# Performance work log

Hardware: AMD Instinct MI355X
Metric: run time of the kernel (lower is better)

## Reference

```python
import jax, jax.numpy as jnp
import numpy as np

B, Cin, Cout, H, W, K = 8, 256, 256, 64, 64, 3  # kernel 3x3, stride 1, pad 1, dilation 1
EPS = 1e-5


def setup_inputs() -> dict:
    key = jax.random.key(0)
    k0, k1, k2 = jax.random.split(key, 3)
    x = jax.random.normal(k0, (B, Cin, H, W), jnp.float32)
    # offset-predicting conv (mmcv zero-inits it; use small random weights so offsets are nontrivial)
    w_off = jax.random.normal(k1, (2 * K * K, Cin, K, K), jnp.float32) * 0.01
    b_off = jnp.zeros((2 * K * K,), jnp.float32)
    # main deformable conv weight
    w = jax.random.normal(k2, (Cout, Cin, K, K), jnp.float32) * (1.0 / np.sqrt(Cin * K * K))
    b = jnp.zeros((Cout,), jnp.float32)
    gamma = jnp.ones((Cout,), jnp.float32)
    beta = jnp.zeros((Cout,), jnp.float32)
    return {"x": x, "w_off": w_off, "b_off": b_off, "w": w, "b": b, "gamma": gamma, "beta": beta}


def _deform_fusion(x, w_off, b_off, w, b, gamma, beta):
    Bn, C, Hh, Ww = x.shape
    # 1) predict offsets: [B, 2*K*K, H, W]; channel layout is (dy, dx) per kernel tap
    offset = jax.lax.conv_general_dilated(x, w_off, (1, 1), ((1, 1), (1, 1)))
    offset = offset + b_off[None, :, None, None]
    off = offset.reshape(Bn, K * K, 2, Hh, Ww)
    dy, dx = off[:, :, 0], off[:, :, 1]  # each [B, K*K, H, W]

    # 2) sampling positions: p = p0 + p_k + delta_p  (stride 1, pad 1 -> p_k in {-1,0,1})
    kk = jnp.arange(K * K)
    ky = (kk // K - (K // 2)).astype(jnp.float32)[None, :, None, None]
    kx = (kk % K - (K // 2)).astype(jnp.float32)[None, :, None, None]
    py = ky + jnp.arange(Hh, dtype=jnp.float32)[None, None, :, None] + dy  # [B,K2,H,W]
    px = kx + jnp.arange(Ww, dtype=jnp.float32)[None, None, None, :] + dx

    # 3) bilinear sampling with zero padding outside the image
    y0 = jnp.floor(py); x0 = jnp.floor(px)
    fy = py - y0; fx = px - x0
    x_flat = x.reshape(Bn, C, Hh * Ww)

    def corner(yi, xi, wgt):
        valid = (yi >= 0) & (yi <= Hh - 1) & (xi >= 0) & (xi <= Ww - 1)
        idx = (jnp.clip(yi, 0, Hh - 1) * Ww + jnp.clip(xi, 0, Ww - 1)).astype(jnp.int32)
        idx = idx.reshape(Bn, -1)  # [B, K2*H*W]
        g = jax.vmap(lambda xf, ii: jnp.take(xf, ii, axis=1))(x_flat, idx)  # [B,C,K2*H*W]
        return g * (wgt * valid).reshape(Bn, 1, -1)

    sampled = (corner(y0,     x0,     (1 - fy) * (1 - fx))
             + corner(y0,     x0 + 1, (1 - fy) * fx)
             + corner(y0 + 1, x0,     fy * (1 - fx))
             + corner(y0 + 1, x0 + 1, fy * fx))  # [B, C, K2*H*W]
    sampled = sampled.reshape(Bn, C, K * K, Hh * Ww)

    # 4) contract sampled patches with conv weight: implicit-GEMM of deformable conv
    out = jnp.einsum('bckp,ock->bop', sampled, w.reshape(w.shape[0], C, K * K))
    out = out + b[None, :, None]
    out = out.reshape(Bn, -1, Hh, Ww)

    # 5) BatchNorm (training-mode batch statistics) + ReLU
    mean = out.mean(axis=(0, 2, 3), keepdims=True)
    var = out.var(axis=(0, 2, 3), keepdims=True)
    out = gamma[None, :, None, None] * (out - mean) * jax.lax.rsqrt(var + EPS) + beta[None, :, None, None]
    return jax.nn.relu(out)


def reference(x, w_off, b_off, w, b, gamma, beta):
    return _deform_fusion(x, w_off, b_off, w, b, gamma, beta)
```

## Files before the change

### kernel.cpp

```cpp
#include <hip/hip_runtime.h>
#include <math.h>

#define BN_ 8
#define CIN 256
#define COUT 256
#define HH 64
#define WW 64
#define HW 4096
#define KK 9
#define OC 18
#define EPS 1e-5f
#define NTOT (BN_ * COUT * HW)

#define OFF_WS 0
#define WTB_WS 589824
#define WOB_WS 884736
#define ST_WS  921600
#define XT_WS  922112

typedef float f32x4 __attribute__((ext_vector_type(4)));
typedef float f32x2 __attribute__((ext_vector_type(2)));
typedef short s16x8 __attribute__((ext_vector_type(8)));
typedef unsigned int u32x4 __attribute__((ext_vector_type(4)));

__device__ __forceinline__ unsigned short f2bf(float f) {
  unsigned int u = __float_as_uint(f);
  unsigned int r = (u + 0x7fffu + ((u >> 16) & 1u)) >> 16;
  return (unsigned short)r;
}
__device__ __forceinline__ float bf2f(short s) {
  return __uint_as_float(((unsigned int)(unsigned short)s) << 16);
}

__global__ __launch_bounds__(256) void xpose_kernel(
    const float* __restrict__ x, unsigned short* __restrict__ xt) {
  __shared__ float s[64][65];
  const int t = threadIdx.x;
  const int p0 = blockIdx.x * 64;
  const int c0 = blockIdx.y * 64;
  const int b  = blockIdx.z;
  const float* xb = x + ((size_t)b * CIN + c0) * HW + p0;
#pragma unroll
  for (int pass = 0; pass < 4; ++pass) {
    int cr = pass * 16 + (t >> 4);
    int ps = (t & 15) * 4;
    float4 v = *(const float4*)(xb + (size_t)cr * HW + ps);
    s[ps + 0][cr] = v.x; s[ps + 1][cr] = v.y; s[ps + 2][cr] = v.z; s[ps + 3][cr] = v.w;
  }
  __syncthreads();
  unsigned short* xo = xt + (size_t)b * 32 * HW * 8;
#pragma unroll
  for (int r = 0; r < 2; ++r) {
    int flat = r * 256 + t;
    int pr = flat >> 3, sub = flat & 7;
    int g8 = (c0 >> 3) + sub;
    s16x8 v;
#pragma unroll
    for (int j = 0; j < 8; ++j) v[j] = (short)f2bf(s[pr][sub * 8 + j]);
    *(s16x8*)(xo + ((size_t)g8 * HW + p0 + pr) * 8) = v;
  }
}

__global__ __launch_bounds__(256) void prep_kernel(
    const float* __restrict__ w_off, const float* __restrict__ w,
    unsigned short* __restrict__ wob, unsigned short* __restrict__ wTb,
    float* __restrict__ stats) {
  const int kb = blockIdx.x;
  const int kk = kb >> 3;
  const int c0 = (kb & 7) << 5;
  const int t = threadIdx.x;
  if (kb == 71) { stats[t] = 0.f; stats[256 + t] = 0.f; }
#pragma unroll
  for (int r = 0; r < 4; ++r) {
    int e = r * 256 + t;
    int g = e >> 8, m = (e >> 3) & 31, j = e & 7;
    int c = c0 + g * 8 + j;
    unsigned short v = 0;
    if (m < OC) v = f2bf(w_off[((size_t)m * CIN + c) * 9 + kk]);
    wob[(size_t)kb * 1024 + e] = v;
  }
#pragma unroll
  for (int g = 0; g < 4; ++g)
#pragma unroll
    for (int j = 0; j < 8; ++j) {
      int c = c0 + g * 8 + j;
      wTb[(((size_t)kb * 4 + g) * 256 + t) * 8 + j] =
          f2bf(w[((size_t)t * CIN + c) * 9 + kk]);
    }
}

__global__ __launch_bounds__(256) void offset_kernel(
    const unsigned short* __restrict__ xt, const unsigned short* __restrict__ wob,
    const float* __restrict__ b_off, float* __restrict__ off_ws) {
  __shared__ __align__(16) char smem[32768];
  const int t = threadIdx.x;
  const int lane = t & 63;
  const int wv = t >> 6;
  const int b = blockIdx.x & 7;
  const int h = blockIdx.x >> 3;
  const unsigned short* xtb = xt + (size_t)b * 32 * HW * 8;
  const int fr = lane & 15, fq = lane >> 4;
  unsigned short* sb = (unsigned short*)smem + wv * 2048;
  float* red = (float*)smem;

  f32x4 acc[2][4] = {};

  for (int s = 0; s < 18; ++s) {
    const int ki = wv * 18 + s;
    const int kk = ki >> 3, cc0 = (ki & 7) << 5;
    const int ky = kk / 3 - 1, kx = kk % 3 - 1;
    const int y = h + ky;
    const bool yok = (y >= 0) && (y < HH);
    const int xcol = lane + kx;
    const bool ok = yok && (xcol >= 0) && (xcol < WW);
    const int pix = y * WW + xcol;

    s16x8 af[2];
    const unsigned short* ap = wob + (size_t)ki * 1024;
#pragma unroll
    for (int i = 0; i < 2; ++i)
      af[i] = *(const s16x8*)&ap[(fq * 32 + i * 16 + fr) * 8];

#pragma unroll
    for (int g = 0; g < 4; ++g) {
      s16x8 v = {0, 0, 0, 0, 0, 0, 0, 0};
      if (ok)
        __builtin_memcpy(&v, (const char*)xtb + ((((size_t)(cc0 >> 3) + g) << 16)) + (size_t)pix * 16, 16);
      *(s16x8*)&sb[(g * 64 + lane) * 8] = v;
    }
    __builtin_amdgcn_s_waitcnt(0);

    s16x8 bf[4];
#pragma unroll
    for (int jn = 0; jn < 4; ++jn)
      bf[jn] = *(const s16x8*)&sb[(fq * 64 + jn * 16 + fr) * 8];
#pragma unroll
    for (int i = 0; i < 2; ++i)
#pragma unroll
      for (int jn = 0; jn < 4; ++jn)
        acc[i][jn] = __builtin_amdgcn_mfma_f32_16x16x32_bf16(af[i], bf[jn], acc[i][jn], 0, 0, 0);
  }

  __syncthreads();
#pragma unroll
  for (int i = 0; i < 2; ++i)
#pragma unroll
    for (int jn = 0; jn < 4; ++jn)
#pragma unroll
      for (int rg = 0; rg < 4; ++rg)
        red[wv * 2048 + (i * 16 + fq * 4 + rg) * 64 + jn * 16 + fr] = acc[i][jn][rg];
  __syncthreads();

  const int m = t >> 3;
  const int pq = (t & 7) * 8;
  float4 v0 = make_float4(0.f, 0.f, 0.f, 0.f), v1 = v0;
#pragma unroll
  for (int w = 0; w < 4; ++w) {
    float4 a = *(float4*)&red[w * 2048 + m * 64 + pq];
    float4 c = *(float4*)&red[w * 2048 + m * 64 + pq + 4];
    v0.x += a.x; v0.y += a.y; v0.z += a.z; v0.w += a.w;
    v1.x += c.x; v1.y += c.y; v1.z += c.z; v1.w += c.w;
  }
  if (m < OC) {
    float bo = b_off[m];
    v0.x += bo; v0.y += bo; v0.z += bo; v0.w += bo;
    v1.x += bo; v1.y += bo; v1.z += bo; v1.w += bo;
    float* op = off_ws + ((size_t)b * OC + m) * HW + h * WW + pq;
    *(float4*)op = v0;
    *(float4*)(op + 4) = v1;
  }
}

__global__ __launch_bounds__(512, 4) void gemm_kernel(
    const unsigned short* __restrict__ xt, const unsigned short* __restrict__ wTb,
    const float* __restrict__ off_ws, const float* __restrict__ bias,
    float* __restrict__ out, float* __restrict__ stats) {
  __shared__ unsigned short s_b[2][4096];
  const int t = threadIdx.x;
  const int lane = t & 63;
  const int wv = t >> 6;
  const int b = blockIdx.x & 7;
  const int h = blockIdx.x >> 3;
  const int p0 = h * 64;
  const int col = t & 63;
  const int oct = t >> 6;
  const int fr = lane & 15, fq = lane >> 4;
  const unsigned short* xtb = xt + (size_t)b * 32 * HW * 8;
  const float* offp = off_ws + (size_t)b * OC * HW + p0 + col;

  int cofs[4];
  f32x2 qw2[4];

  auto calc = [&](int kk, float dy, float dx) {
    float py = (float)(kk / 3 - 1 + h) + dy;
    float pxx = (float)(kk % 3 - 1 + col) + dx;
    float y0f = floorf(py), x0f = floorf(pxx);
    float fy = py - y0f, fx = pxx - x0f;
    int y0 = (int)y0f, x0 = (int)x0f;
    int y1 = y0 + 1, x1 = x0 + 1;
    bool vy0 = (y0 >= 0) && (y0 < HH), vy1 = (y1 >= 0) && (y1 < HH);
    bool vx0 = (x0 >= 0) && (x0 < WW), vx1 = (x1 >= 0) && (x1 < WW);
    int cy0 = min(max(y0, 0), HH - 1), cy1 = min(max(y1, 0), HH - 1);
    int cx0 = min(max(x0, 0), WW - 1), cx1 = min(max(x1, 0), WW - 1);
    float q0 = (vy0 && vx0) ? (1.f - fy) * (1.f - fx) : 0.f;
    float q1 = (vy0 && vx1) ? (1.f - fy) * fx : 0.f;
    float q2 = (vy1 && vx0) ? fy * (1.f - fx) : 0.f;
    float q3 = (vy1 && vx1) ? fy * fx : 0.f;
    cofs[0] = (cy0 * WW + cx0) * 16;  qw2[0][0] = q0; qw2[0][1] = q0;
    cofs[1] = (cy0 * WW + cx1) * 16;  qw2[1][0] = q1; qw2[1][1] = q1;
    cofs[2] = (cy1 * WW + cx0) * 16;  qw2[2][0] = q2; qw2[2][1] = q2;
    cofs[3] = (cy1 * WW + cx1) * 16;  qw2[3][0] = q3; qw2[3][1] = q3;
  };

  s16x8 g[4];

  auto gather = [&](int chunk64) {
    const char* bp = (const char*)xtb + (((size_t)(chunk64 * 8 + oct)) << 16);
#pragma unroll
    for (int k = 0; k < 4; ++k)
      __builtin_memcpy(&g[k], bp + cofs[k], 16);
  };

  auto combine_write = [&](int buf) {
    u32x4 vout;
#pragma unroll
    for (int jp = 0; jp < 4; ++jp) {
      f32x2 a = {0.f, 0.f};
#pragma unroll
      for (int k = 0; k < 4; ++k) {
        unsigned int pr = ((const unsigned int*)&g[k])[jp];
        f32x2 xv;
        xv[0] = __uint_as_float(pr << 16);
        xv[1] = __uint_as_float(pr & 0xffff0000u);
        a = __builtin_elementwise_fma(qw2[k], xv, a);
      }
      unsigned int packed;
      asm("v_cvt_pk_bf16_f32 %0, %1, %2" : "=v"(packed) : "v"(a[0]), "v"(a[1]));
      vout[jp] = packed;
    }
    *(u32x4*)&s_b[buf][(oct * 64 + col) * 8] = vout;
  };

  auto load_a = [&](int iter, s16x8 af[2][2]) {
#pragma unroll
    for (int ks = 0; ks < 2; ++ks) {
      const unsigned short* ap =
          wTb + (((size_t)(iter * 2 + ks) * 4 + fq) * 256 + wv * 32 + fr) * 8;
#pragma unroll
      for (int i = 0; i < 2; ++i)
        af[ks][i] = *(const s16x8*)(ap + (size_t)i * 16 * 8);
    }
  };

  f32x4 acc[2][4] = {};
  s16x8 afE[2][2], afO[2][2];
  float dyp, dxp;

  {
    float dy0 = offp[0];
    float dx0 = offp[HW];
    calc(0, dy0, dx0);
    dyp = offp[2 * HW];
    dxp = offp[3 * HW];
    gather(0);
    load_a(0, afE);
    combine_write(0);
  }
  asm volatile("s_waitcnt lgkmcnt(0)" ::: "memory");
  __builtin_amdgcn_s_barrier();

#define GBODY(I, AFC, AFN, CUR)                                                \
  {                                                                            \
    const int nx1 = (I) + 1;                                                   \
    if (nx1 < 36) {                                                            \
      if ((nx1 & 3) == 0) {                                                    \
        const int kkc = nx1 >> 2;                                              \
        calc(kkc, dyp, dxp);                                                   \
        const int kkn = kkc + 1;                                               \
        if (kkn < 9) {                                                         \
          dyp = offp[(size_t)(2 * kkn) * HW];                                  \
          dxp = offp[(size_t)(2 * kkn + 1) * HW];                              \
        }                                                                      \
      }                                                                        \
      gather(nx1 & 3);                                                         \
      load_a(nx1, AFN);                                                        \
    }                                                                          \
    __builtin_amdgcn_s_setprio(1);                                             \
    _Pragma("unroll")                                                          \
    for (int ks = 0; ks < 2; ++ks)                                             \
      _Pragma("unroll")                                                        \
      for (int jj = 0; jj < 4; ++jj) {                                         \
        s16x8 bfr = *(const s16x8*)&s_b[CUR][((ks * 4 + fq) * 64 + jj * 16 + fr) * 8]; \
        _Pragma("unroll")                                                      \
        for (int ii = 0; ii < 2; ++ii)                                         \
          acc[ii][jj] = __builtin_amdgcn_mfma_f32_16x16x32_bf16(               \
              AFC[ks][ii], bfr, acc[ii][jj], 0, 0, 0);                         \
      }                                                                        \
    __builtin_amdgcn_s_setprio(0);                                             \
    if (nx1 < 36) {                                                            \
      combine_write((CUR) ^ 1);                                                \
      asm volatile("s_waitcnt lgkmcnt(0)" ::: "memory");                       \
      __builtin_amdgcn_s_barrier();                                            \
    }                                                                          \
  }

  for (int m = 0; m < 18; ++m) {
    const int i0 = 2 * m;
    GBODY(i0, afE, afO, 0)
    GBODY(i0 + 1, afO, afE, 1)
  }
#undef GBODY

#pragma unroll
  for (int i = 0; i < 2; ++i) {
#pragma unroll
    for (int rg = 0; rg < 4; ++rg) {
      int o = wv * 32 + i * 16 + fq * 4 + rg;
      float bv = bias[o];
      float* op = out + ((size_t)(b * COUT + o)) * HW + p0 + fr;
      float s = 0.f, s2 = 0.f;
#pragma unroll
      for (int j = 0; j < 4; ++j) {
        float val = acc[i][j][rg] + bv;
        op[j * 16] = val;
        s += val; s2 += val * val;
      }
#pragma unroll
      for (int m2 = 1; m2 < 16; m2 <<= 1) {
        s += __shfl_xor(s, m2);
        s2 += __shfl_xor(s2, m2);
      }
      if (fr == 0) {
        atomicAdd(&stats[o], s);
        atomicAdd(&stats[COUT + o], s2);
      }
    }
  }
}

__global__ __launch_bounds__(256) void bn_kernel(
    float* __restrict__ out, const float* __restrict__ stats,
    const float* __restrict__ gamma, const float* __restrict__ beta) {
  int i4 = (blockIdx.x * 256 + threadIdx.x) * 4;
  int o = (i4 >> 12) & (COUT - 1);
  const float inv_n = 1.f / (float)(BN_ * HW);
  float mean = stats[o] * inv_n;
  float var = stats[COUT + o] * inv_n - mean * mean;
  float sc = gamma[o] * rsqrtf(var + EPS);
  float sh = beta[o] - mean * sc;
  float4 v = *(float4*)(out + i4);
  v.x = fmaxf(fmaf(v.x, sc, sh), 0.f);
  v.y = fmaxf(fmaf(v.y, sc, sh), 0.f);
  v.z = fmaxf(fmaf(v.z, sc, sh), 0.f);
  v.w = fmaxf(fmaf(v.w, sc, sh), 0.f);
  *(float4*)(out + i4) = v;
}

extern "C" void kernel_launch(void* const* d_in, const int* in_sizes, int n_in,
                              void* d_out, int out_size, void* d_ws, size_t ws_size,
                              hipStream_t stream) {
  const float* x     = (const float*)d_in[0];
  const float* w_off = (const float*)d_in[1];
  const float* b_off = (const float*)d_in[2];
  const float* w     = (const float*)d_in[3];
  const float* bias  = (const float*)d_in[4];
  const float* gamma = (const float*)d_in[5];
  const float* beta  = (const float*)d_in[6];
  float* out = (float*)d_out;
  float* ws = (float*)d_ws;
  float* off_ws = ws + OFF_WS;
  unsigned short* wTb = (unsigned short*)(ws + WTB_WS);
  unsigned short* wob = (unsigned short*)(ws + WOB_WS);
  float* stats = ws + ST_WS;
  unsigned short* xt = (unsigned short*)(ws + XT_WS);

  xpose_kernel<<<dim3(64, 4, 8), 256, 0, stream>>>(x, xt);
  prep_kernel<<<72, 256, 0, stream>>>(w_off, w, wob, wTb, stats);
  offset_kernel<<<512, 256, 0, stream>>>(xt, wob, b_off, off_ws);
  gemm_kernel<<<512, 512, 0, stream>>>(xt, wTb, off_ws, bias, out, stats);
  bn_kernel<<<NTOT / 1024, 256, 0, stream>>>(out, stats, gamma, beta);
}
```

Before: 221.3 us.

## Warp-specialize GEMM kernel into MFMA consumer waves and gather producer waves

Splits the 8 waves of each block into 4 compute waves, which run the MFMA loop with a larger 64-row tile each, and 4 producer waves, which do the bilinear gather and bf16 packing into the double-buffered LDS tile. Previously every wave both gathered and computed. The aim is to overlap the irregular gather latency with matrix work through producer/consumer specialization. In exchange, each compute wave holds twice the accumulators and A fragments, which raises register pressure, and each producer handles two channel slots.

```diff
diff --git a/kernel.cpp b/kernel.cpp
--- a/kernel.cpp
+++ b/kernel.cpp
@@ -182,158 +182,164 @@
   const int b = blockIdx.x & 7;
   const int h = blockIdx.x >> 3;
   const int p0 = h * 64;
-  const int col = t & 63;
-  const int oct = t >> 6;
   const int fr = lane & 15, fq = lane >> 4;
   const unsigned short* xtb = xt + (size_t)b * 32 * HW * 8;
-  const float* offp = off_ws + (size_t)b * OC * HW + p0 + col;
-
-  int cofs[4];
-  f32x2 qw2[4];
-
-  auto calc = [&](int kk, float dy, float dx) {
-    float py = (float)(kk / 3 - 1 + h) + dy;
-    float pxx = (float)(kk % 3 - 1 + col) + dx;
-    float y0f = floorf(py), x0f = floorf(pxx);
-    float fy = py - y0f, fx = pxx - x0f;
-    int y0 = (int)y0f, x0 = (int)x0f;
-    int y1 = y0 + 1, x1 = x0 + 1;
-    bool vy0 = (y0 >= 0) && (y0 < HH), vy1 = (y1 >= 0) && (y1 < HH);
-    bool vx0 = (x0 >= 0) && (x0 < WW), vx1 = (x1 >= 0) && (x1 < WW);
-    int cy0 = min(max(y0, 0), HH - 1), cy1 = min(max(y1, 0), HH - 1);
-    int cx0 = min(max(x0, 0), WW - 1), cx1 = min(max(x1, 0), WW - 1);
-    float q0 = (vy0 && vx0) ? (1.f - fy) * (1.f - fx) : 0.f;
-    float q1 = (vy0 && vx1) ? (1.f - fy) * fx : 0.f;
-    float q2 = (vy1 && vx0) ? fy * (1.f - fx) : 0.f;
-    float q3 = (vy1 && vx1) ? fy * fx : 0.f;
-    cofs[0] = (cy0 * WW + cx0) * 16;  qw2[0][0] = q0; qw2[0][1] = q0;
-    cofs[1] = (cy0 * WW + cx1) * 16;  qw2[1][0] = q1; qw2[1][1] = q1;
-    cofs[2] = (cy1 * WW + cx0) * 16;  qw2[2][0] = q2; qw2[2][1] = q2;
-    cofs[3] = (cy1 * WW + cx1) * 16;  qw2[3][0] = q3; qw2[3][1] = q3;
-  };
-
-  s16x8 g[4];
-
-  auto gather = [&](int chunk64) {
-    const char* bp = (const char*)xtb + (((size_t)(chunk64 * 8 + oct)) << 16);
-#pragma unroll
-    for (int k = 0; k < 4; ++k)
-      __builtin_memcpy(&g[k], bp + cofs[k], 16);
-  };
-
-  auto combine_write = [&](int buf) {
-    u32x4 vout;
-#pragma unroll
-    for (int jp = 0; jp < 4; ++jp) {
-      f32x2 a = {0.f, 0.f};
+
+  if (wv < 4) {
+    f32x4 acc[4][4] = {};
+    s16x8 af[2][4];
+
+    auto load_af = [&](int iter) {
+#pragma unroll
+      for (int ks = 0; ks < 2; ++ks) {
+        const unsigned short* ap =
+            wTb + (((size_t)(iter * 2 + ks) * 4 + fq) * 256 + wv * 64 + fr) * 8;
+#pragma unroll
+        for (int i = 0; i < 4; ++i)
+          af[ks][i] = *(const s16x8*)(ap + (size_t)i * 16 * 8);
+      }
+    };
+
+    load_af(0);
+    asm volatile("s_waitcnt lgkmcnt(0)" ::: "memory");
+    __builtin_amdgcn_s_barrier();
+
+    for (int I = 0; I < 36; ++I) {
+      const int cur = I & 1;
+      __builtin_amdgcn_s_setprio(1);
+#pragma unroll
+      for (int ks = 0; ks < 2; ++ks)
+#pragma unroll
+        for (int jj = 0; jj < 4; ++jj) {
+          s16x8 bfr = *(const s16x8*)&s_b[cur][((ks * 4 + fq) * 64 + jj * 16 + fr) * 8];
+#pragma unroll
+          for (int ii = 0; ii < 4; ++ii)
+            acc[ii][jj] = __builtin_amdgcn_mfma_f32_16x16x32_bf16(
+                af[ks][ii], bfr, acc[ii][jj], 0, 0, 0);
+        }
+      __builtin_amdgcn_s_setprio(0);
+      if (I + 1 < 36) load_af(I + 1);
+      asm volatile("s_waitcnt lgkmcnt(0)" ::: "memory");
+      __builtin_amdgcn_s_barrier();
+    }
+
+#pragma unroll
+    for (int i = 0; i < 4; ++i) {
+#pragma unroll
+      for (int rg = 0; rg < 4; ++rg) {
+        int o = wv * 64 + i * 16 + fq * 4 + rg;
+        float bv = bias[o];
+        float* op = out + ((size_t)(b * COUT + o)) * HW + p0 + fr;
+        float s = 0.f, s2 = 0.f;
+#pragma unroll
+        for (int j = 0; j < 4; ++j) {
+          float val = acc[i][j][rg] + bv;
+          op[j * 16] = val;
+          s += val; s2 += val * val;
+        }
+#pragma unroll
+        for (int m2 = 1; m2 < 16; m2 <<= 1) {
+          s += __shfl_xor(s, m2);
+          s2 += __shfl_xor(s2, m2);
+        }
+        if (fr == 0) {
+          atomicAdd(&stats[o], s);
+          atomicAdd(&stats[COUT + o], s2);
+        }
+      }
+    }
+  } else {
+    const int col = lane;
+    const int octp = wv & 3;
+    const float* offp = off_ws + (size_t)b * OC * HW + p0 + col;
+
+    int cofs[4];
+    f32x2 qw2[4];
+    s16x8 g[2][4];
+
+    auto calc = [&](int kk, float dy, float dx) {
+      float py = (float)(kk / 3 - 1 + h) + dy;
+      float pxx = (float)(kk % 3 - 1 + col) + dx;
+      float y0f = floorf(py), x0f = floorf(pxx);
+      float fy = py - y0f, fx = pxx - x0f;
+      int y0 = (int)y0f, x0 = (int)x0f;
+      int y1 = y0 + 1, x1 = x0 + 1;
+      bool vy0 = (y0 >= 0) && (y0 < HH), vy1 = (y1 >= 0) && (y1 < HH);
+      bool vx0 = (x0 >= 0) && (x0 < WW), vx1 = (x1 >= 0) && (x1 < WW);
+      int cy0 = min(max(y0, 0), HH - 1), cy1 = min(max(y1, 0), HH - 1);
+      int cx0 = min(max(x0, 0), WW - 1), cx1 = min(max(x1, 0), WW - 1);
+      float q0 = (vy0 && vx0) ? (1.f - fy) * (1.f - fx) : 0.f;
+      float q1 = (vy0 && vx1) ? (1.f - fy) * fx : 0.f;
+      float q2 = (vy1 && vx0) ? fy * (1.f - fx) : 0.f;
+      float q3 = (vy1 && vx1) ? fy * fx : 0.f;
+      cofs[0] = (cy0 * WW + cx0) * 16;  qw2[0][0] = q0; qw2[0][1] = q0;
+      cofs[1] = (cy0 * WW + cx1) * 16;  qw2[1][0] = q1; qw2[1][1] = q1;
+      cofs[2] = (cy1 * WW + cx0) * 16;  qw2[2][0] = q2; qw2[2][1] = q2;
+      cofs[3] = (cy1 * WW + cx1) * 16;  qw2[3][0] = q3; qw2[3][1] = q3;
+    };
+
+    auto gather = [&](int chunk64) {
+      const char* bp0 = (const char*)xtb + (((size_t)(chunk64 * 8 + octp * 2)) << 16);
 #pragma unroll
       for (int k = 0; k < 4; ++k) {
-        unsigned int pr = ((const unsigned int*)&g[k])[jp];
-        f32x2 xv;
-        xv[0] = __uint_as_float(pr << 16);
-        xv[1] = __uint_as_float(pr & 0xffff0000u);
-        a = __builtin_elementwise_fma(qw2[k], xv, a);
-      }
-      unsigned int packed;
-      asm("v_cvt_pk_bf16_f32 %0, %1, %2" : "=v"(packed) : "v"(a[0]), "v"(a[1]));
-      vout[jp] = packed;
-    }
-    *(u32x4*)&s_b[buf][(oct * 64 + col) * 8] = vout;
-  };
-
-  auto load_a = [&](int iter, s16x8 af[2][2]) {
-#pragma unroll
-    for (int ks = 0; ks < 2; ++ks) {
-      const unsigned short* ap =
-          wTb + (((size_t)(iter * 2 + ks) * 4 + fq) * 256 + wv * 32 + fr) * 8;
-#pragma unroll
-      for (int i = 0; i < 2; ++i)
-        af[ks][i] = *(const s16x8*)(ap + (size_t)i * 16 * 8);
-    }
-  };
-
-  f32x4 acc[2][4] = {};
-  s16x8 afE[2][2], afO[2][2];
-  float dyp, dxp;
-
-  {
-    float dy0 = offp[0];
-    float dx0 = offp[HW];
-    calc(0, dy0, dx0);
-    dyp = offp[2 * HW];
-    dxp = offp[3 * HW];
-    gather(0);
-    load_a(0, afE);
-    combine_write(0);
-  }
-  asm volatile("s_waitcnt lgkmcnt(0)" ::: "memory");
-  __builtin_amdgcn_s_barrier();
-
-#define GBODY(I, AFC, AFN, CUR)                                                \
-  {                                                                            \
-    const int nx1 = (I) + 1;                                                   \
-    if (nx1 < 36) {                                                            \
-      if ((nx1 & 3) == 0) {                                                    \
-        const int kkc = nx1 >> 2;                                              \
-        calc(kkc, dyp, dxp);                                                   \
-        const int kkn = kkc + 1;                                               \
-        if (kkn < 9) {                                                         \
-          dyp = offp[(size_t)(2 * kkn) * HW];                                  \
-          dxp = offp[(size_t)(2 * kkn + 1) * HW];                              \
-        }                                                                      \
-      }                                                                        \
-      gather(nx1 & 3);                                                         \
-      load_a(nx1, AFN);                                                        \
-    }                                                                          \
-    __builtin_amdgcn_s_setprio(1);                                             \
-    _Pragma("unroll")                                                          \
-    for (int ks = 0; ks < 2; ++ks)                                             \
-      _Pragma("unroll")                                                        \
-      for (int jj = 0; jj < 4; ++jj) {                                         \
-        s16x8 bfr = *(const s16x8*)&s_b[CUR][((ks * 4 + fq) * 64 + jj * 16 + fr) * 8]; \
-        _Pragma("unroll")                                                      \
-        for (int ii = 0; ii < 2; ++ii)                                         \
-          acc[ii][jj] = __builtin_amdgcn_mfma_f32_16x16x32_bf16(               \
-              AFC[ks][ii], bfr, acc[ii][jj], 0, 0, 0);                         \
-      }                                                                        \
-    __builtin_amdgcn_s_setprio(0);                                             \
-    if (nx1 < 36) {                                                            \
-      combine_write((CUR) ^ 1);                                                \
-      asm volatile("s_waitcnt lgkmcnt(0)" ::: "memory");                       \
-      __builtin_amdgcn_s_barrier();                                            \
-    }                                                                          \
-  }
-
-  for (int m = 0; m < 18; ++m) {
-    const int i0 = 2 * m;
-    GBODY(i0, afE, afO, 0)
-    GBODY(i0 + 1, afO, afE, 1)
-  }
-#undef GBODY
-
-#pragma unroll
-  for (int i = 0; i < 2; ++i) {
-#pragma unroll
-    for (int rg = 0; rg < 4; ++rg) {
-      int o = wv * 32 + i * 16 + fq * 4 + rg;
-      float bv = bias[o];
-      float* op = out + ((size_t)(b * COUT + o)) * HW + p0 + fr;
-      float s = 0.f, s2 = 0.f;
-#pragma unroll
-      for (int j = 0; j < 4; ++j) {
-        float val = acc[i][j][rg] + bv;
-        op[j * 16] = val;
-        s += val; s2 += val * val;
-      }
-#pragma unroll
-      for (int m2 = 1; m2 < 16; m2 <<= 1) {
-        s += __shfl_xor(s, m2);
-        s2 += __shfl_xor(s2, m2);
-      }
-      if (fr == 0) {
-        atomicAdd(&stats[o], s);
-        atomicAdd(&stats[COUT + o], s2);
-      }
+        __builtin_memcpy(&g[0][k], bp0 + cofs[k], 16);
+        __builtin_memcpy(&g[1][k], bp0 + (1 << 16) + cofs[k], 16);
+      }
+    };
+
+    auto combine_write = [&](int buf) {
+#pragma unroll
+      for (int slot = 0; slot < 2; ++slot) {
+        u32x4 vout;
+#pragma unroll
+        for (int jp = 0; jp < 4; ++jp) {
+          f32x2 a = {0.f, 0.f};
+#pragma unroll
+          for (int k = 0; k < 4; ++k) {
+            unsigned int pr = ((const unsigned int*)&g[slot][k])[jp];
+            f32x2 xv;
+            xv[0] = __uint_as_float(pr << 16);
+            xv[1] = __uint_as_float(pr & 0xffff0000u);
+            a = __builtin_elementwise_fma(qw2[k], xv, a);
+          }
+          unsigned int packed;
+          asm("v_cvt_pk_bf16_f32 %0, %1, %2" : "=v"(packed) : "v"(a[0]), "v"(a[1]));
+          vout[jp] = packed;
+        }
+        *(u32x4*)&s_b[buf][((octp * 2 + slot) * 64 + col) * 8] = vout;
+      }
+    };
+
+    float dyp, dxp;
+    {
+      float dy0 = offp[0];
+      float dx0 = offp[HW];
+      calc(0, dy0, dx0);
+      dyp = offp[2 * HW];
+      dxp = offp[3 * HW];
+      gather(0);
+      combine_write(0);
+    }
+    asm volatile("s_waitcnt lgkmcnt(0)" ::: "memory");
+    __builtin_amdgcn_s_barrier();
+
+    for (int I = 0; I < 36; ++I) {
+      const int nx1 = I + 1;
+      if (nx1 < 36) {
+        if ((nx1 & 3) == 0) {
+          const int kkc = nx1 >> 2;
+          calc(kkc, dyp, dxp);
+          const int kkn = kkc + 1;
+          if (kkn < 9) {
+            dyp = offp[(size_t)(2 * kkn) * HW];
+            dxp = offp[(size_t)(2 * kkn + 1) * HW];
+          }
+        }
+        gather(nx1 & 3);
+        combine_write((I & 1) ^ 1);
+      }
+      asm volatile("s_waitcnt lgkmcnt(0)" ::: "memory");
+      __builtin_amdgcn_s_barrier();
     }
   }
 }
```

Result: no change. 223.5 us (+1.0%).

## Fuse BatchNorm+ReLU into GEMM via grid barrier; prefetch offset-conv operands

Applied to the files above, without the earlier changes.

The separate bn_kernel pass is removed. The GEMM kernel now accumulates per-channel statistics, waits on a software grid-wide barrier (an atomic counter placed in a padding slot of the offset-weight buffer), and then applies the normalisation, bias and ReLU directly to its register accumulators before the only store of the output. This avoids writing the pre-BN output and then reading and rewriting it. The offset kernel is also software-pipelined: the global loads for the next step are issued before the current step's LDS reads and MFMAs. The barrier assumes all 512 blocks are resident at once, and it relies on prep_kernel resetting the padding slot on every call.

```diff
diff --git a/kernel.cpp b/kernel.cpp
--- a/kernel.cpp
+++ b/kernel.cpp
@@ -105,41 +105,53 @@
 
   f32x4 acc[2][4] = {};
 
-  for (int s = 0; s < 18; ++s) {
+  auto fetch = [&](int s, s16x8* V, s16x8* AF) {
     const int ki = wv * 18 + s;
-    const int kk = ki >> 3, cc0 = (ki & 7) << 5;
+    const int kk = ki >> 3, cc0g = (ki & 7) << 2;
     const int ky = kk / 3 - 1, kx = kk % 3 - 1;
     const int y = h + ky;
-    const bool yok = (y >= 0) && (y < HH);
     const int xcol = lane + kx;
-    const bool ok = yok && (xcol >= 0) && (xcol < WW);
+    const bool ok = (y >= 0) && (y < HH) && (xcol >= 0) && (xcol < WW);
     const int pix = y * WW + xcol;
-
-    s16x8 af[2];
-    const unsigned short* ap = wob + (size_t)ki * 1024;
-#pragma unroll
-    for (int i = 0; i < 2; ++i)
-      af[i] = *(const s16x8*)&ap[(fq * 32 + i * 16 + fr) * 8];
-
 #pragma unroll
     for (int g = 0; g < 4; ++g) {
       s16x8 v = {0, 0, 0, 0, 0, 0, 0, 0};
       if (ok)
-        __builtin_memcpy(&v, (const char*)xtb + ((((size_t)(cc0 >> 3) + g) << 16)) + (size_t)pix * 16, 16);
-      *(s16x8*)&sb[(g * 64 + lane) * 8] = v;
-    }
-    __builtin_amdgcn_s_waitcnt(0);
-
-    s16x8 bf[4];
-#pragma unroll
-    for (int jn = 0; jn < 4; ++jn)
-      bf[jn] = *(const s16x8*)&sb[(fq * 64 + jn * 16 + fr) * 8];
+        __builtin_memcpy(&v, (const char*)xtb + (((size_t)(cc0g + g)) << 16) + (size_t)pix * 16, 16);
+      V[g] = v;
+    }
+    const unsigned short* ap = wob + (size_t)ki * 1024;
 #pragma unroll
     for (int i = 0; i < 2; ++i)
-#pragma unroll
-      for (int jn = 0; jn < 4; ++jn)
-        acc[i][jn] = __builtin_amdgcn_mfma_f32_16x16x32_bf16(af[i], bf[jn], acc[i][jn], 0, 0, 0);
-  }
+      AF[i] = *(const s16x8*)&ap[(fq * 32 + i * 16 + fr) * 8];
+  };
+
+  s16x8 VE[4], VO[4], afE[2], afO[2];
+  fetch(0, VE, afE);
+
+#define OBODY(S, VC, VN, AFC, AFN)                                             \
+  {                                                                            \
+    _Pragma("unroll")                                                          \
+    for (int g = 0; g < 4; ++g)                                                \
+      *(s16x8*)&sb[(g * 64 + lane) * 8] = VC[g];                               \
+    if ((S) + 1 < 18) fetch((S) + 1, VN, AFN);                                 \
+    s16x8 bf[4];                                                               \
+    _Pragma("unroll")                                                          \
+    for (int jn = 0; jn < 4; ++jn)                                             \
+      bf[jn] = *(const s16x8*)&sb[(fq * 64 + jn * 16 + fr) * 8];               \
+    _Pragma("unroll")                                                          \
+    for (int i = 0; i < 2; ++i)                                                \
+      _Pragma("unroll")                                                        \
+      for (int jn = 0; jn < 4; ++jn)                                           \
+        acc[i][jn] = __builtin_amdgcn_mfma_f32_16x16x32_bf16(                  \
+            AFC[i], bf[jn], acc[i][jn], 0, 0, 0);                              \
+  }
+
+  for (int sp = 0; sp < 9; ++sp) {
+    OBODY(2 * sp, VE, VO, afE, afO)
+    OBODY(2 * sp + 1, VO, VE, afO, afE)
+  }
+#undef OBODY
 
   __syncthreads();
 #pragma unroll
@@ -174,7 +186,9 @@
 __global__ __launch_bounds__(512, 4) void gemm_kernel(
     const unsigned short* __restrict__ xt, const unsigned short* __restrict__ wTb,
     const float* __restrict__ off_ws, const float* __restrict__ bias,
-    float* __restrict__ out, float* __restrict__ stats) {
+    const float* __restrict__ gamma, const float* __restrict__ beta,
+    float* __restrict__ out, float* __restrict__ stats,
+    unsigned int* __restrict__ bar) {
   __shared__ unsigned short s_b[2][4096];
   const int t = threadIdx.x;
   const int lane = t & 63;
@@ -312,17 +326,15 @@
 #undef GBODY
 
 #pragma unroll
-  for (int i = 0; i < 2; ++i) {
+  for (int i = 0; i < 2; ++i)
 #pragma unroll
     for (int rg = 0; rg < 4; ++rg) {
       int o = wv * 32 + i * 16 + fq * 4 + rg;
       float bv = bias[o];
-      float* op = out + ((size_t)(b * COUT + o)) * HW + p0 + fr;
       float s = 0.f, s2 = 0.f;
 #pragma unroll
       for (int j = 0; j < 4; ++j) {
         float val = acc[i][j][rg] + bv;
-        op[j * 16] = val;
         s += val; s2 += val * val;
       }
 #pragma unroll
@@ -335,25 +347,32 @@
         atomicAdd(&stats[COUT + o], s2);
       }
     }
-  }
-}
-
-__global__ __launch_bounds__(256) void bn_kernel(
-    float* __restrict__ out, const float* __restrict__ stats,
-    const float* __restrict__ gamma, const float* __restrict__ beta) {
-  int i4 = (blockIdx.x * 256 + threadIdx.x) * 4;
-  int o = (i4 >> 12) & (COUT - 1);
+
+  __syncthreads();
+  if (t == 0) {
+    atomicAdd(bar, 1u);
+    while (atomicOr(bar, 0u) < 512u) __builtin_amdgcn_s_sleep(2);
+  }
+  __syncthreads();
+
+  float* s_stats = (float*)s_b;
+  s_stats[t] = __hip_atomic_load(&stats[t], __ATOMIC_RELAXED, __HIP_MEMORY_SCOPE_AGENT);
+  __syncthreads();
   const float inv_n = 1.f / (float)(BN_ * HW);
-  float mean = stats[o] * inv_n;
-  float var = stats[COUT + o] * inv_n - mean * mean;
-  float sc = gamma[o] * rsqrtf(var + EPS);
-  float sh = beta[o] - mean * sc;
-  float4 v = *(float4*)(out + i4);
-  v.x = fmaxf(fmaf(v.x, sc, sh), 0.f);
-  v.y = fmaxf(fmaf(v.y, sc, sh), 0.f);
-  v.z = fmaxf(fmaf(v.z, sc, sh), 0.f);
-  v.w = fmaxf(fmaf(v.w, sc, sh), 0.f);
-  *(float4*)(out + i4) = v;
+#pragma unroll
+  for (int i = 0; i < 2; ++i)
+#pragma unroll
+    for (int rg = 0; rg < 4; ++rg) {
+      int o = wv * 32 + i * 16 + fq * 4 + rg;
+      float mean = s_stats[o] * inv_n;
+      float var = s_stats[COUT + o] * inv_n - mean * mean;
+      float sc = gamma[o] * rsqrtf(var + EPS);
+      float sh = beta[o] - mean * sc + bias[o] * sc;
+      float* op = out + ((size_t)(b * COUT + o)) * HW + p0 + fr;
+#pragma unroll
+      for (int j = 0; j < 4; ++j)
+        op[j * 16] = fmaxf(fmaf(acc[i][j][rg], sc, sh), 0.f);
+    }
 }
 
 extern "C" void kernel_launch(void* const* d_in, const int* in_sizes, int n_in,
@@ -373,10 +392,10 @@
   unsigned short* wob = (unsigned short*)(ws + WOB_WS);
   float* stats = ws + ST_WS;
   unsigned short* xt = (unsigned short*)(ws + XT_WS);
+  unsigned int* bar = (unsigned int*)(wob + (size_t)71 * 1024 + 1016);
 
   xpose_kernel<<<dim3(64, 4, 8), 256, 0, stream>>>(x, xt);
   prep_kernel<<<72, 256, 0, stream>>>(w_off, w, wob, wTb, stats);
   offset_kernel<<<512, 256, 0, stream>>>(xt, wob, b_off, off_ws);
-  gemm_kernel<<<512, 512, 0, stream>>>(xt, wTb, off_ws, bias, out, stats);
-  bn_kernel<<<NTOT / 1024, 256, 0, stream>>>(out, stats, gamma, beta);
-}
+  gemm_kernel<<<512, 512, 0, stream>>>(xt, wTb, off_ws, bias, gamma, beta, out, stats, bar);
+}
```

Result: no change. 225.3 us (+1.8%).

## Fuse offset-prediction conv into deformable GEMM kernel via shared-memory offsets

Applied to the files above, without the earlier changes.

Removes the separate offset_kernel and computes the 18-channel offset conv for each row tile at the start of gemm_kernel, using 8 waves (9 steps each) with register double-buffered fetches. Offsets are stored in LDS rather than a global workspace, which eliminates one launch and the global write and read-back of the offsets. The cost is a larger LDS footprint (72KB per block), which may lower occupancy for the launch_bounds(512,4) GEMM, and a serialized prologue before the main GEMM starts.

```diff
diff --git a/kernel.cpp b/kernel.cpp
--- a/kernel.cpp
+++ b/kernel.cpp
@@ -89,93 +89,12 @@
     }
 }
 
-__global__ __launch_bounds__(256) void offset_kernel(
-    const unsigned short* __restrict__ xt, const unsigned short* __restrict__ wob,
-    const float* __restrict__ b_off, float* __restrict__ off_ws) {
-  __shared__ __align__(16) char smem[32768];
-  const int t = threadIdx.x;
-  const int lane = t & 63;
-  const int wv = t >> 6;
-  const int b = blockIdx.x & 7;
-  const int h = blockIdx.x >> 3;
-  const unsigned short* xtb = xt + (size_t)b * 32 * HW * 8;
-  const int fr = lane & 15, fq = lane >> 4;
-  unsigned short* sb = (unsigned short*)smem + wv * 2048;
-  float* red = (float*)smem;
-
-  f32x4 acc[2][4] = {};
-
-  for (int s = 0; s < 18; ++s) {
-    const int ki = wv * 18 + s;
-    const int kk = ki >> 3, cc0 = (ki & 7) << 5;
-    const int ky = kk / 3 - 1, kx = kk % 3 - 1;
-    const int y = h + ky;
-    const bool yok = (y >= 0) && (y < HH);
-    const int xcol = lane + kx;
-    const bool ok = yok && (xcol >= 0) && (xcol < WW);
-    const int pix = y * WW + xcol;
-
-    s16x8 af[2];
-    const unsigned short* ap = wob + (size_t)ki * 1024;
-#pragma unroll
-    for (int i = 0; i < 2; ++i)
-      af[i] = *(const s16x8*)&ap[(fq * 32 + i * 16 + fr) * 8];
-
-#pragma unroll
-    for (int g = 0; g < 4; ++g) {
-      s16x8 v = {0, 0, 0, 0, 0, 0, 0, 0};
-      if (ok)
-        __builtin_memcpy(&v, (const char*)xtb + ((((size_t)(cc0 >> 3) + g) << 16)) + (size_t)pix * 16, 16);
-      *(s16x8*)&sb[(g * 64 + lane) * 8] = v;
-    }
-    __builtin_amdgcn_s_waitcnt(0);
-
-    s16x8 bf[4];
-#pragma unroll
-    for (int jn = 0; jn < 4; ++jn)
-      bf[jn] = *(const s16x8*)&sb[(fq * 64 + jn * 16 + fr) * 8];
-#pragma unroll
-    for (int i = 0; i < 2; ++i)
-#pragma unroll
-      for (int jn = 0; jn < 4; ++jn)
-        acc[i][jn] = __builtin_amdgcn_mfma_f32_16x16x32_bf16(af[i], bf[jn], acc[i][jn], 0, 0, 0);
-  }
-
-  __syncthreads();
-#pragma unroll
-  for (int i = 0; i < 2; ++i)
-#pragma unroll
-    for (int jn = 0; jn < 4; ++jn)
-#pragma unroll
-      for (int rg = 0; rg < 4; ++rg)
-        red[wv * 2048 + (i * 16 + fq * 4 + rg) * 64 + jn * 16 + fr] = acc[i][jn][rg];
-  __syncthreads();
-
-  const int m = t >> 3;
-  const int pq = (t & 7) * 8;
-  float4 v0 = make_float4(0.f, 0.f, 0.f, 0.f), v1 = v0;
-#pragma unroll
-  for (int w = 0; w < 4; ++w) {
-    float4 a = *(float4*)&red[w * 2048 + m * 64 + pq];
-    float4 c = *(float4*)&red[w * 2048 + m * 64 + pq + 4];
-    v0.x += a.x; v0.y += a.y; v0.z += a.z; v0.w += a.w;
-    v1.x += c.x; v1.y += c.y; v1.z += c.z; v1.w += c.w;
-  }
-  if (m < OC) {
-    float bo = b_off[m];
-    v0.x += bo; v0.y += bo; v0.z += bo; v0.w += bo;
-    v1.x += bo; v1.y += bo; v1.z += bo; v1.w += bo;
-    float* op = off_ws + ((size_t)b * OC + m) * HW + h * WW + pq;
-    *(float4*)op = v0;
-    *(float4*)(op + 4) = v1;
-  }
-}
-
 __global__ __launch_bounds__(512, 4) void gemm_kernel(
     const unsigned short* __restrict__ xt, const unsigned short* __restrict__ wTb,
-    const float* __restrict__ off_ws, const float* __restrict__ bias,
-    float* __restrict__ out, float* __restrict__ stats) {
-  __shared__ unsigned short s_b[2][4096];
+    const unsigned short* __restrict__ wob, const float* __restrict__ b_off,
+    const float* __restrict__ bias, float* __restrict__ out,
+    float* __restrict__ stats) {
+  __shared__ __align__(16) char lds[73728];
   const int t = threadIdx.x;
   const int lane = t & 63;
   const int wv = t >> 6;
@@ -186,12 +105,93 @@
   const int oct = t >> 6;
   const int fr = lane & 15, fq = lane >> 4;
   const unsigned short* xtb = xt + (size_t)b * 32 * HW * 8;
-  const float* offp = off_ws + (size_t)b * OC * HW + p0 + col;
+  float* s_off = (float*)(lds + 65536);
+  unsigned short (*s_b)[4096] = (unsigned short(*)[4096])lds;
+
+  {
+    unsigned short* sb = (unsigned short*)lds + wv * 2048;
+    f32x4 acc_o[2][4] = {};
+
+    auto fetch = [&](int s, s16x8* V, s16x8* AF) {
+      const int ki = wv * 9 + s;
+      const int kk = ki >> 3, cc0g = (ki & 7) << 2;
+      const int ky = kk / 3 - 1, kx = kk % 3 - 1;
+      const int y = h + ky;
+      const int xcol = lane + kx;
+      const bool ok = (y >= 0) && (y < HH) && (xcol >= 0) && (xcol < WW);
+      const int pix = y * WW + xcol;
+#pragma unroll
+      for (int g = 0; g < 4; ++g) {
+        s16x8 v = {0, 0, 0, 0, 0, 0, 0, 0};
+        if (ok)
+          __builtin_memcpy(&v, (const char*)xtb + (((size_t)(cc0g + g)) << 16) + (size_t)pix * 16, 16);
+        V[g] = v;
+      }
+      const unsigned short* ap = wob + (size_t)ki * 1024;
+#pragma unroll
+      for (int i = 0; i < 2; ++i)
+        AF[i] = *(const s16x8*)&ap[(fq * 32 + i * 16 + fr) * 8];
+    };
+
+    s16x8 VE[4], VO[4], afE2[2], afO2[2];
+    fetch(0, VE, afE2);
+
+#define OBODY(S, VC, VN, AFC, AFN)                                             \
+    {                                                                          \
+      _Pragma("unroll")                                                        \
+      for (int g = 0; g < 4; ++g)                                              \
+        *(s16x8*)&sb[(g * 64 + lane) * 8] = VC[g];                             \
+      if ((S) + 1 < 9) fetch((S) + 1, VN, AFN);                                \
+      s16x8 bf[4];                                                             \
+      _Pragma("unroll")                                                        \
+      for (int jn = 0; jn < 4; ++jn)                                           \
+        bf[jn] = *(const s16x8*)&sb[(fq * 64 + jn * 16 + fr) * 8];             \
+      _Pragma("unroll")                                                        \
+      for (int i = 0; i < 2; ++i)                                              \
+        _Pragma("unroll")                                                      \
+        for (int jn = 0; jn < 4; ++jn)                                         \
+          acc_o[i][jn] = __builtin_amdgcn_mfma_f32_16x16x32_bf16(              \
+              AFC[i], bf[jn], acc_o[i][jn], 0, 0, 0);                          \
+    }
+
+    for (int sp = 0; sp < 4; ++sp) {
+      OBODY(2 * sp, VE, VO, afE2, afO2)
+      OBODY(2 * sp + 1, VO, VE, afO2, afE2)
+    }
+    OBODY(8, VE, VO, afE2, afO2)
+#undef OBODY
+
+    __syncthreads();
+    float* red = (float*)lds;
+#pragma unroll
+    for (int i = 0; i < 2; ++i)
+#pragma unroll
+      for (int jn = 0; jn < 4; ++jn)
+#pragma unroll
+        for (int rg = 0; rg < 4; ++rg)
+          red[wv * 2048 + (i * 16 + fq * 4 + rg) * 64 + jn * 16 + fr] = acc_o[i][jn][rg];
+    __syncthreads();
+
+    const int e4 = t * 4;
+    const int m = e4 >> 6;
+    float4 v = make_float4(0.f, 0.f, 0.f, 0.f);
+#pragma unroll
+    for (int w = 0; w < 8; ++w) {
+      float4 a = *(float4*)&red[w * 2048 + e4];
+      v.x += a.x; v.y += a.y; v.z += a.z; v.w += a.w;
+    }
+    float bo = (m < OC) ? b_off[m] : 0.f;
+    v.x += bo; v.y += bo; v.z += bo; v.w += bo;
+    *(float4*)&s_off[e4] = v;
+    __syncthreads();
+  }
 
   int cofs[4];
   f32x2 qw2[4];
 
-  auto calc = [&](int kk, float dy, float dx) {
+  auto calc = [&](int kk) {
+    float dy = s_off[(2 * kk) * 64 + col];
+    float dx = s_off[(2 * kk + 1) * 64 + col];
     float py = (float)(kk / 3 - 1 + h) + dy;
     float pxx = (float)(kk % 3 - 1 + col) + dx;
     float y0f = floorf(py), x0f = floorf(pxx);
@@ -254,14 +254,9 @@
 
   f32x4 acc[2][4] = {};
   s16x8 afE[2][2], afO[2][2];
-  float dyp, dxp;
 
   {
-    float dy0 = offp[0];
-    float dx0 = offp[HW];
-    calc(0, dy0, dx0);
-    dyp = offp[2 * HW];
-    dxp = offp[3 * HW];
+    calc(0);
     gather(0);
     load_a(0, afE);
     combine_write(0);
@@ -273,15 +268,7 @@
   {                                                                            \
     const int nx1 = (I) + 1;                                                   \
     if (nx1 < 36) {                                                            \
-      if ((nx1 & 3) == 0) {                                                    \
-        const int kkc = nx1 >> 2;                                              \
-        calc(kkc, dyp, dxp);                                                   \
-        const int kkn = kkc + 1;                                               \
-        if (kkn < 9) {                                                         \
-          dyp = offp[(size_t)(2 * kkn) * HW];                                  \
-          dxp = offp[(size_t)(2 * kkn + 1) * HW];                              \
-        }                                                                      \
-      }                                                                        \
+      if ((nx1 & 3) == 0) calc(nx1 >> 2);                                      \
       gather(nx1 & 3);                                                         \
       load_a(nx1, AFN);                                                        \
     }                                                                          \
@@ -368,7 +355,6 @@
   const float* beta  = (const float*)d_in[6];
   float* out = (float*)d_out;
   float* ws = (float*)d_ws;
-  float* off_ws = ws + OFF_WS;
   unsigned short* wTb = (unsigned short*)(ws + WTB_WS);
   unsigned short* wob = (unsigned short*)(ws + WOB_WS);
   float* stats = ws + ST_WS;
@@ -376,7 +362,6 @@
 
   xpose_kernel<<<dim3(64, 4, 8), 256, 0, stream>>>(x, xt);
   prep_kernel<<<72, 256, 0, stream>>>(w_off, w, wob, wTb, stats);
-  offset_kernel<<<512, 256, 0, stream>>>(xt, wob, b_off, off_ws);
-  gemm_kernel<<<512, 512, 0, stream>>>(xt, wTb, off_ws, bias, out, stats);
+  gemm_kernel<<<512, 512, 0, stream>>>(xt, wTb, wob, b_off, bias, out, stats);
   bn_kernel<<<NTOT / 1024, 256, 0, stream>>>(out, stats, gamma, beta);
 }
```

Result: faster. 213.7 us (-3.4%).
